# Optimization experiments

Hardware: AMD Instinct MI355X
Metric: run time of the kernel (lower is better)

The kernel has to match this reference:

```python
import jax, jax.numpy as jnp
import numpy as np

N_NODES = 10000
K_HOPS = 2
PICKS = 4       # random out-edges per node before symmetrization (~8 avg degree)
D_MAX = 128     # pad width for k-hop neighborhoods
BATCH = 2
F_DIM = 64


def _build_neighborhoods(n, k_hops, picks, d_max, seed=0):
    """Random sparse graph; returns padded k-hop neighborhood indices + lengths.
    Mirrors graphTools.computeNeighborhood: hop-k set = nodes reachable in <=k
    hops, including the node itself."""
    rng = np.random.default_rng(seed)
    nbrs = [set() for _ in range(n)]
    for u in range(n):
        for v in rng.integers(0, n, size=picks):
            v = int(v)
            if v != u:
                nbrs[u].add(v)
                nbrs[v].add(u)
    hop = [{u} | nbrs[u] for u in range(n)]  # 1-hop (incl. self)
    one_hop = hop
    idx = np.empty((k_hops, n, d_max), dtype=np.int32)
    lens = np.empty((k_hops, n), dtype=np.int32)
    for k in range(k_hops):
        if k > 0:
            hop = [set().union(*(one_hop[m] for m in hop[u])) for u in range(n)]
        for u in range(n):
            nb = sorted(hop[u])[:d_max]  # clip (never hit for this graph)
            lens[k, u] = len(nb)
            idx[k, u, :len(nb)] = nb
            idx[k, u, len(nb):] = u  # pad with self (masked out anyway)
    return idx, lens


def setup_inputs() -> dict:
    key = jax.random.key(0)
    kx, kw = jax.random.split(key)
    x = jax.random.normal(kx, (BATCH, F_DIM, N_NODES), dtype=jnp.float32)
    stdv = 1.0 / np.sqrt(K_HOPS)
    weight = jax.random.uniform(kw, (1, K_HOPS + 1), minval=-stdv, maxval=stdv,
                                dtype=jnp.float32)
    idx, lens = _build_neighborhoods(N_NODES, K_HOPS, PICKS, D_MAX)
    return {"x": x, "weight": weight,
            "neigh_idx": jnp.asarray(idx), "neigh_len": jnp.asarray(lens)}


def _masked_median(x, idx, ln):
    # x: [B,F,N]; idx: [N,D]; ln: [N] -> lower median over each ragged set,
    # matching torch.median (element at sorted position (len-1)//2).
    D = idx.shape[1]
    vals = x[:, :, idx]                                   # [B,F,N,D] gather
    mask = jnp.arange(D, dtype=ln.dtype)[None, :] < ln[:, None]  # [N,D]
    vals = jnp.where(mask[None, None], vals, jnp.inf)
    vals = jnp.sort(vals, axis=-1)
    mid = ((ln - 1) // 2).astype(jnp.int32)               # [N]
    med = jnp.take_along_axis(vals, mid[None, None, :, None], axis=-1)
    return med[..., 0]                                    # [B,F,N]


def reference(x, weight, neigh_idx, neigh_len):
    K = neigh_idx.shape[0]
    hops = [x] + [_masked_median(x, neigh_idx[k], neigh_len[k]) for k in range(K)]
    xK = jnp.stack(hops, axis=-1)                         # [B,F,N,K+1]
    return jnp.einsum('bfnk,k->bfn', xK, weight[0])
```

## Files before the change

### kernel.cpp

```cpp
#include <hip/hip_runtime.h>
#include <hip/hip_bf16.h>

constexpr int NN   = 10000;
constexpr int DMAX = 128;
constexpr int ROWS = 128;

__global__ __launch_bounds__(256) void transpose_kernel(
    const float* __restrict__ x, float* __restrict__ xT)
{
    __shared__ float tile[32][33];
    const int n0 = blockIdx.x * 32;
    const int r0 = blockIdx.y * 32;
    const int tx = threadIdx.x;
    const int ty = threadIdx.y;
    #pragma unroll
    for (int i = 0; i < 32; i += 8) {
        const int r = r0 + ty + i;
        const int n = n0 + tx;
        if (n < NN) tile[ty + i][tx] = x[(size_t)r * NN + n];
    }
    __syncthreads();
    #pragma unroll
    for (int i = 0; i < 32; i += 8) {
        const int n = n0 + ty + i;
        const int r = r0 + tx;
        if (n < NN) xT[(size_t)n * ROWS + r] = tile[tx][ty + i];
    }
}

template<int QC>
__device__ __forceinline__ float median_sel(const float* __restrict__ xT,
                                            const int* __restrict__ idxp,
                                            int ln, int col, int half)
{
    const float INF = 1e30f;
    float data[QC];
    #pragma unroll
    for (int j = 0; j < QC; ++j) {
        const int  jj    = half * QC + j;
        const bool valid = jj < ln;
        const int  nb    = valid ? idxp[jj] : 0;
        const float v    = xT[(nb << 7) + col];
        data[j] = valid ? v : INF;
    }

    const int   mid  = (ln - 1) >> 1;
    const float midf = (float)mid + 0.5f;
    const float invs = 1.0f / (0.4f * (float)ln);
    float lo = -64.f, hi = 64.f, m = 0.f, x = 0.f;
    float mp = 0.f, cpf = 0.f;
    bool active = true, need_snap = false, have_prev = false;
    int  pass = 0;

    while (__ballot(active) != 0ull) {
        const bool dosnap = (pass >= 3) || (__ballot(need_snap) != 0ull);

        int   cA = 0, cB = 0, cC = 0, cD = 0;
        float mx0 = -INF, mx1 = -INF, mn0 = INF, mn1 = INF;
        if (dosnap) {
            #pragma unroll
            for (int j = 0; j < QC; j += 4) {
                const float v0 = data[j], v1 = data[j+1],
                            v2 = data[j+2], v3 = data[j+3];
                const bool l0 = v0 <= m, l1 = v1 <= m,
                           l2 = v2 <= m, l3 = v3 <= m;
                cA += l0; cB += l1; cC += l2; cD += l3;
                mx0 = l0 ? fmaxf(mx0, v0) : mx0;  mn0 = l0 ? mn0 : fminf(mn0, v0);
                mx1 = l1 ? fmaxf(mx1, v1) : mx1;  mn1 = l1 ? mn1 : fminf(mn1, v1);
                mx0 = l2 ? fmaxf(mx0, v2) : mx0;  mn0 = l2 ? mn0 : fminf(mn0, v2);
                mx1 = l3 ? fmaxf(mx1, v3) : mx1;  mn1 = l3 ? mn1 : fminf(mn1, v3);
            }
        } else {
            #pragma unroll
            for (int j = 0; j < QC; j += 4) {
                cA += data[j]   <= m;  cB += data[j+1] <= m;
                cC += data[j+2] <= m;  cD += data[j+3] <= m;
            }
        }
        int c = (cA + cB) + (cC + cD);
        c += __shfl_xor(c, 32);
        float mx = fmaxf(mx0, mx1), mn = fminf(mn0, mn1);
        if (dosnap) {
            mx = fmaxf(mx, __shfl_xor(mx, 32));
            mn = fminf(mn, __shfl_xor(mn, 32));
        }

        if (active) {
            const float fc = (float)c;
            if (dosnap) {
                need_snap = false;
                if      (c == mid + 1) { x = mx; active = false; }
                else if (c == mid)     { x = mn; active = false; }
                else {
                    if (c > mid + 1) hi = mx; else lo = mn;
                    if (lo >= hi) { x = lo; active = false; }
                    else {
                        const float dd = fc - cpf;
                        float mN = (have_prev && dd != 0.f)
                                 ? m + (midf - fc) * (m - mp) * __builtin_amdgcn_rcpf(dd)
                                 : m + (midf - fc) * invs;
                        mp = m; cpf = fc; have_prev = true;
                        if (!(mN > lo && mN < hi)) mN = 0.5f * (lo + hi);
                        if (mN >= hi) mN = lo;
                        m = mN;
                    }
                }
            } else {
                if (c == mid + 1 || c == mid) {
                    need_snap = true;
                } else {
                    if (c > mid + 1) hi = m; else lo = m;
                    const float dd = fc - cpf;
                    float mN = (have_prev && dd != 0.f)
                             ? m + (midf - fc) * (m - mp) * __builtin_amdgcn_rcpf(dd)
                             : m + (midf - fc) * invs;
                    mp = m; cpf = fc; have_prev = true;
                    if (!(mN > lo && mN < hi)) mN = 0.5f * (lo + hi);
                    if (mN >= hi) mN = lo;
                    m = mN;
                }
            }
        }
        ++pass;
    }
    return x;
}

__device__ __forceinline__ float median_dispatch(const float* __restrict__ xT,
                                                 const int* __restrict__ idxp,
                                                 int ln, int col, int half)
{
    if (ln <= 16)  return median_sel< 8>(xT, idxp, ln, col, half);
    if (ln <= 32)  return median_sel<16>(xT, idxp, ln, col, half);
    if (ln <= 48)  return median_sel<24>(xT, idxp, ln, col, half);
    if (ln <= 64)  return median_sel<32>(xT, idxp, ln, col, half);
    if (ln <= 80)  return median_sel<40>(xT, idxp, ln, col, half);
    if (ln <= 96)  return median_sel<48>(xT, idxp, ln, col, half);
    if (ln <= 112) return median_sel<56>(xT, idxp, ln, col, half);
    return median_sel<64>(xT, idxp, ln, col, half);
}

__global__ __launch_bounds__(256, 4) void median_combine(
    const float* __restrict__ xT, const float* __restrict__ w,
    const int* __restrict__ nidx, const int* __restrict__ nlen,
    float* __restrict__ out)
{
    const int t    = threadIdx.x;
    const int wv   = t >> 6;
    const int l    = t & 63;
    const int col  = (wv << 5) | (l & 31);
    const int half = l >> 5;
    const int n    = blockIdx.x;

    float medk[2];
    #pragma unroll
    for (int k = 0; k < 2; ++k) {
        const int ln = nlen[k * NN + n];
        const int* idxp = nidx + ((size_t)k * NN + n) * DMAX;
        medk[k] = median_dispatch(xT, idxp, ln, col, half);
    }

    if (half == 0) {
        const float xv = xT[(n << 7) + col];
        out[col * NN + n] = w[0] * xv + w[1] * medk[0] + w[2] * medk[1];
    }
}

extern "C" void kernel_launch(void* const* d_in, const int* in_sizes, int n_in,
                              void* d_out, int out_size, void* d_ws, size_t ws_size,
                              hipStream_t stream) {
    const float* x    = (const float*)d_in[0];
    const float* w    = (const float*)d_in[1];
    const int*   nidx = (const int*)d_in[2];
    const int*   nlen = (const int*)d_in[3];
    float* out = (float*)d_out;
    float* xT  = (float*)d_ws;

    dim3 tb(32, 8);
    dim3 tg((NN + 31) / 32, ROWS / 32);
    transpose_kernel<<<tg, tb, 0, stream>>>(x, xT);
    median_combine<<<NN, 256, 0, stream>>>(xT, w, nidx, nlen, out);
}
```

Before: 356.6 us.

## Split each median column across four lane groups instead of two

Each column's neighbor set is now spread over 4 lanes (16 columns per wave) instead of 2, so each lane holds a quarter of the values. Blocks now cover 64 columns, and twice as many blocks are launched. The aim is fewer registers per lane and shorter per-lane count loops, giving more parallelism and occupancy. In exchange, every pass needs an extra cross-lane shuffle, and the 16-lane groups read from global memory in narrower contiguous segments.

```diff
diff --git a/kernel.cpp b/kernel.cpp
--- a/kernel.cpp
+++ b/kernel.cpp
@@ -31,13 +31,13 @@
 template<int QC>
 __device__ __forceinline__ float median_sel(const float* __restrict__ xT,
                                             const int* __restrict__ idxp,
-                                            int ln, int col, int half)
+                                            int ln, int col, int q)
 {
     const float INF = 1e30f;
     float data[QC];
     #pragma unroll
     for (int j = 0; j < QC; ++j) {
-        const int  jj    = half * QC + j;
+        const int  jj    = q * QC + j;
         const bool valid = jj < ln;
         const int  nb    = valid ? idxp[jj] : 0;
         const float v    = xT[(nb << 7) + col];
@@ -55,33 +55,31 @@
     while (__ballot(active) != 0ull) {
         const bool dosnap = (pass >= 3) || (__ballot(need_snap) != 0ull);
 
-        int   cA = 0, cB = 0, cC = 0, cD = 0;
+        int   cA = 0, cB = 0;
         float mx0 = -INF, mx1 = -INF, mn0 = INF, mn1 = INF;
         if (dosnap) {
             #pragma unroll
-            for (int j = 0; j < QC; j += 4) {
-                const float v0 = data[j], v1 = data[j+1],
-                            v2 = data[j+2], v3 = data[j+3];
-                const bool l0 = v0 <= m, l1 = v1 <= m,
-                           l2 = v2 <= m, l3 = v3 <= m;
-                cA += l0; cB += l1; cC += l2; cD += l3;
+            for (int j = 0; j < QC; j += 2) {
+                const float v0 = data[j], v1 = data[j + 1];
+                const bool  l0 = v0 <= m, l1 = v1 <= m;
+                cA += l0; cB += l1;
                 mx0 = l0 ? fmaxf(mx0, v0) : mx0;  mn0 = l0 ? mn0 : fminf(mn0, v0);
                 mx1 = l1 ? fmaxf(mx1, v1) : mx1;  mn1 = l1 ? mn1 : fminf(mn1, v1);
-                mx0 = l2 ? fmaxf(mx0, v2) : mx0;  mn0 = l2 ? mn0 : fminf(mn0, v2);
-                mx1 = l3 ? fmaxf(mx1, v3) : mx1;  mn1 = l3 ? mn1 : fminf(mn1, v3);
             }
         } else {
             #pragma unroll
-            for (int j = 0; j < QC; j += 4) {
-                cA += data[j]   <= m;  cB += data[j+1] <= m;
-                cC += data[j+2] <= m;  cD += data[j+3] <= m;
+            for (int j = 0; j < QC; j += 2) {
+                cA += data[j] <= m;  cB += data[j + 1] <= m;
             }
         }
-        int c = (cA + cB) + (cC + cD);
+        int c = cA + cB;
+        c += __shfl_xor(c, 16);
         c += __shfl_xor(c, 32);
         float mx = fmaxf(mx0, mx1), mn = fminf(mn0, mn1);
         if (dosnap) {
+            mx = fmaxf(mx, __shfl_xor(mx, 16));
             mx = fmaxf(mx, __shfl_xor(mx, 32));
+            mn = fminf(mn, __shfl_xor(mn, 16));
             mn = fminf(mn, __shfl_xor(mn, 32));
         }
 
@@ -128,16 +126,16 @@
 
 __device__ __forceinline__ float median_dispatch(const float* __restrict__ xT,
                                                  const int* __restrict__ idxp,
-                                                 int ln, int col, int half)
+                                                 int ln, int col, int q)
 {
-    if (ln <= 16)  return median_sel< 8>(xT, idxp, ln, col, half);
-    if (ln <= 32)  return median_sel<16>(xT, idxp, ln, col, half);
-    if (ln <= 48)  return median_sel<24>(xT, idxp, ln, col, half);
-    if (ln <= 64)  return median_sel<32>(xT, idxp, ln, col, half);
-    if (ln <= 80)  return median_sel<40>(xT, idxp, ln, col, half);
-    if (ln <= 96)  return median_sel<48>(xT, idxp, ln, col, half);
-    if (ln <= 112) return median_sel<56>(xT, idxp, ln, col, half);
-    return median_sel<64>(xT, idxp, ln, col, half);
+    if (ln <= 16)  return median_sel< 4>(xT, idxp, ln, col, q);
+    if (ln <= 32)  return median_sel< 8>(xT, idxp, ln, col, q);
+    if (ln <= 48)  return median_sel<12>(xT, idxp, ln, col, q);
+    if (ln <= 64)  return median_sel<16>(xT, idxp, ln, col, q);
+    if (ln <= 80)  return median_sel<20>(xT, idxp, ln, col, q);
+    if (ln <= 96)  return median_sel<24>(xT, idxp, ln, col, q);
+    if (ln <= 112) return median_sel<28>(xT, idxp, ln, col, q);
+    return median_sel<32>(xT, idxp, ln, col, q);
 }
 
 __global__ __launch_bounds__(256, 4) void median_combine(
@@ -145,22 +143,23 @@
     const int* __restrict__ nidx, const int* __restrict__ nlen,
     float* __restrict__ out)
 {
-    const int t    = threadIdx.x;
-    const int wv   = t >> 6;
-    const int l    = t & 63;
-    const int col  = (wv << 5) | (l & 31);
-    const int half = l >> 5;
-    const int n    = blockIdx.x;
+    const int t   = threadIdx.x;
+    const int wv  = t >> 6;
+    const int l   = t & 63;
+    const int g   = l & 15;
+    const int q   = l >> 4;
+    const int n   = blockIdx.x >> 1;
+    const int col = ((blockIdx.x & 1) << 6) | (wv << 4) | g;
 
     float medk[2];
     #pragma unroll
     for (int k = 0; k < 2; ++k) {
         const int ln = nlen[k * NN + n];
         const int* idxp = nidx + ((size_t)k * NN + n) * DMAX;
-        medk[k] = median_dispatch(xT, idxp, ln, col, half);
+        medk[k] = median_dispatch(xT, idxp, ln, col, q);
     }
 
-    if (half == 0) {
+    if (q == 0) {
         const float xv = xT[(n << 7) + col];
         out[col * NN + n] = w[0] * xv + w[1] * medk[0] + w[2] * medk[1];
     }
@@ -179,5 +178,5 @@
     dim3 tb(32, 8);
     dim3 tg((NN + 31) / 32, ROWS / 32);
     transpose_kernel<<<tg, tb, 0, stream>>>(x, xT);
-    median_combine<<<NN, 256, 0, stream>>>(xT, w, nidx, nlen, out);
+    median_combine<<<NN * 2, 256, 0, stream>>>(xT, w, nidx, nlen, out);
 }
```

Result: slower. 378.2 us (+6.1%).
